# Kernel tuning notes

Measured on AMD Instinct MI355X. Metric: run time of the kernel, lower is better.

The kernel has to match this reference:

```python
import jax, jax.numpy as jnp
import numpy as np

NUM_PTS = 4
N_OFF = 4


def inverse_sigmoid(x, eps=1e-5):
    x = jnp.clip(x, 0.0, 1.0)
    return jnp.log(jnp.clip(x, eps, None) / jnp.clip(1.0 - x, eps, None))


def uniform_flat_indices(T, H, W, n):
    # torch: linspace(hop/2, D-1-hop/2, n).round().long(), meshed over (t,h,w)
    def ax(D):
        hop = D / n
        return jnp.round(jnp.linspace(hop / 2.0, D - 1.0 - hop / 2.0, n)).astype(jnp.int32)
    ti, hi, wi = ax(T), ax(H), ax(W)
    return ((ti[:, None, None] * H + hi[None, :, None]) * W + wi[None, None, :]).reshape(-1)


def _normalized_thw(idx, T, H, W):
    wn = (idx % W).astype(jnp.float32) / (W - 1)
    hn = ((idx // W) % H).astype(jnp.float32) / (H - 1)
    tn = (idx // (W * H)).astype(jnp.float32) / (T - 1)
    return jnp.stack([tn, hn, wn], axis=-1)


def grid_sample_3d(inp, grid):
    # Matches torch F.grid_sample 5D, bilinear, padding zeros, align_corners=False.
    # inp: (N,C,D,H,W); grid: (N,Do,Ho,Wo,3) with grid[...,0]=x->W, 1=y->H, 2=z->D
    N, C, D, H, W = inp.shape
    Do, Ho, Wo = grid.shape[1:4]
    P = Do * Ho * Wo
    g = grid.reshape(N, P, 3)
    ix = ((g[..., 0] + 1.0) * W - 1.0) * 0.5
    iy = ((g[..., 1] + 1.0) * H - 1.0) * 0.5
    iz = ((g[..., 2] + 1.0) * D - 1.0) * 0.5
    x0 = jnp.floor(ix); y0 = jnp.floor(iy); z0 = jnp.floor(iz)
    fx = ix - x0; fy = iy - y0; fz = iz - z0
    x0i = x0.astype(jnp.int32); y0i = y0.astype(jnp.int32); z0i = z0.astype(jnp.int32)
    inp_flat = inp.reshape(N, C, D * H * W)
    out = jnp.zeros((N, C, P), inp.dtype)
    for dz in (0, 1):
        for dy in (0, 1):
            for dx in (0, 1):
                xi = x0i + dx; yi = y0i + dy; zi = z0i + dz
                w = (fx if dx else 1.0 - fx) * (fy if dy else 1.0 - fy) * (fz if dz else 1.0 - fz)
                valid = (xi >= 0) & (xi < W) & (yi >= 0) & (yi < H) & (zi >= 0) & (zi < D)
                flat = (jnp.clip(zi, 0, D - 1) * H + jnp.clip(yi, 0, H - 1)) * W + jnp.clip(xi, 0, W - 1)
                vals = jnp.take_along_axis(inp_flat, jnp.broadcast_to(flat[:, None, :], (N, C, P)), axis=2)
                out = out + vals * (w * valid.astype(inp.dtype))[:, None, :]
    return out.reshape(N, C, Do, Ho, Wo)


def forward(features, pos, W1, b1, W2, b2, Wn, bn, Wl, bl, Woff, boff, Ww, bw, gamma, beta):
    B, C, T, H, Wd, L = features.shape
    THW = T * H * Wd
    No = N_OFF
    N = NUM_PTS ** 3
    d = C // No
    BLNo = B * L * No

    flat = uniform_flat_indices(T, H, Wd, NUM_PTS)                    # (N,)
    ind_pts = jnp.broadcast_to(flat[None, None, :], (B, L, N))

    feats_l = jnp.transpose(features, (0, 5, 2, 3, 4, 1)).reshape(B, L, THW, C)
    pos_l = jnp.transpose(pos, (0, 5, 2, 3, 4, 1)).reshape(B, L, THW, C)
    sampled_pts = feats_l[:, :, flat, :]                              # (B,L,N,C)
    sampled_pos = pos_l[:, :, flat, :]
    glob = jnp.transpose(jnp.mean(features, axis=(2, 3, 4)), (0, 2, 1))  # (B,L,C)
    glob = jnp.broadcast_to(glob[:, :, None, :], (B, L, N, C))

    off_src = jnp.concatenate([sampled_pts, sampled_pos, glob], axis=-1)
    off_src = jax.nn.relu(off_src @ W1 + b1)
    off_src = jax.nn.relu(off_src @ W2 + b2)                          # (B,L,N,C)

    nxt = off_src @ Wn + bn                                           # (B,L,N,3)
    w_l = jax.nn.softmax(off_src @ Wl + bl, axis=-1)                  # (B,L,N,L)

    osr = off_src.reshape(B, L, N, No, d).transpose(0, 1, 3, 2, 4).reshape(BLNo, N, d)
    offset = osr @ Woff + boff                                        # (BLNo,N,3)
    w_o = jax.nn.softmax(osr @ Ww + bw, axis=-1)[..., 1:]             # (BLNo,N,1)

    # --- build flow field: identity grid with sampled coords scattered in ---
    idx = jnp.broadcast_to(ind_pts[:, :, None, :], (B, L, No, N)).reshape(BLNo, N)
    thw = _normalized_thw(idx, T, H, Wd)
    samp = jax.nn.sigmoid(inverse_sigmoid(thw) + offset) * 2.0 - 1.0  # (BLNo,N,3)
    mesh = jnp.stack(jnp.meshgrid(jnp.linspace(-1.0, 1.0, T), jnp.linspace(-1.0, 1.0, H), jnp.linspace(-1.0, 1.0, Wd), indexing='ij'), axis=-1).reshape(THW, 3)
    base = jnp.broadcast_to(mesh[None], (BLNo, THW, 3))
    bI = jnp.arange(BLNo)[:, None]
    flow = base.at[bI, idx].set(samp).reshape(BLNo, T, H, Wd, 3)

    feats_rep = jnp.transpose(features, (0, 5, 1, 2, 3, 4))           # (B,L,C,T,H,W)
    feats_rep = jnp.broadcast_to(feats_rep[:, :, None], (B, L, No, C, T, H, Wd)).reshape(BLNo, C, T, H, Wd)
    sf = grid_sample_3d(feats_rep, flow)                              # (BLNo,C,T,H,W)
    sf = jnp.transpose(sf, (0, 2, 3, 4, 1))                           # (BLNo,T,H,W,C)

    wo_full = jnp.zeros((BLNo, THW, 1), features.dtype).at[bI, idx].set(w_o).reshape(BLNo, T, H, Wd, 1)
    wsf = (sf * wo_full).reshape(B, L, No, T, H, Wd, C).sum(axis=2)   # (B,L,T,H,W,C)
    feats2 = features + jnp.transpose(wsf, (0, 5, 2, 3, 4, 1))        # (B,C,T,H,W,L)

    # level weights scattered then summed over target-level axis l
    bI2 = jnp.arange(B)[:, None, None]
    lI2 = jnp.arange(L)[None, :, None]
    wl_full = jnp.zeros((B, L, THW, L), features.dtype).at[bI2, lI2, ind_pts].set(w_l)
    wl_sum = wl_full.sum(axis=-1).reshape(B, L, T, H, Wd)             # (B,L,T,H,W)
    feats3 = feats2 * jnp.transpose(wl_sum, (0, 2, 3, 4, 1))[:, None] # broadcast over C

    # LayerNorm over channel dim (transpose(1,-1) in torch)
    x = jnp.transpose(feats3, (0, 5, 2, 3, 4, 1))                     # (B,L,T,H,W,C)
    mu = jnp.mean(x, axis=-1, keepdims=True)
    var = jnp.var(x, axis=-1, keepdims=True)
    xn = (x - mu) * jax.lax.rsqrt(var + 1e-5) * gamma + beta
    feats_out = jnp.transpose(xn, (0, 5, 2, 3, 4, 1))

    # offset_adder -> next flattened indices
    thw2 = _normalized_thw(ind_pts, T, H, Wd)
    disp = jax.nn.sigmoid(inverse_sigmoid(thw2) + nxt)
    scale = jnp.array([T - 1, H - 1, Wd - 1], jnp.float32)
    di = jnp.round(disp * scale).astype(jnp.int32)
    next_ind = H * Wd * di[..., 0] + Wd * di[..., 1] + di[..., 2]
    return feats_out, next_ind


def setup_inputs():
    key = jax.random.key(0)
    ks = jax.random.split(key, 10)
    B, C, T, H, W, L = 1, 256, 8, 32, 32, 4
    s = 0.02
    d = C // N_OFF
    return {
        'features': jax.random.normal(ks[0], (B, C, T, H, W, L), jnp.float32),
        'pos': jax.random.normal(ks[1], (B, C, T, H, W, L), jnp.float32),
        'W1': jax.random.normal(ks[2], (3 * C, C), jnp.float32) * s,
        'b1': jnp.zeros((C,), jnp.float32),
        'W2': jax.random.normal(ks[3], (C, C), jnp.float32) * s,
        'b2': jnp.zeros((C,), jnp.float32),
        'Wn': jax.random.normal(ks[4], (C, 3), jnp.float32) * s,
        'bn': jnp.zeros((3,), jnp.float32),
        'Wl': jax.random.normal(ks[5], (C, L), jnp.float32) * s,
        'bl': jnp.zeros((L,), jnp.float32),
        'Woff': jax.random.normal(ks[6], (d, 3), jnp.float32) * s,
        'boff': jnp.zeros((3,), jnp.float32),
        'Ww': jax.random.normal(ks[7], (d, 2), jnp.float32) * s,
        'bw': jnp.zeros((2,), jnp.float32),
        'gamma': jnp.ones((C,), jnp.float32),
        'beta': jnp.zeros((C,), jnp.float32),
    }


def reference(features, pos, W1, b1, W2, b2, Wn, bn, Wl, bl, Woff, boff, Ww, bw, gamma, beta):
    return forward(features, pos, W1, b1, W2, b2, Wn, bn, Wl, bl, Woff, boff, Ww, bw, gamma, beta)
```

## Files before the change

### kernel.cpp

```cpp
#include <hip/hip_runtime.h>
#include <math.h>

#define CDIM 256
#define TDIM 8
#define HDIM 32
#define WDIM 32
#define LDIM 4
#define THW 8192
#define CSTR 32768
#define NS 64
#define OUT0_SIZE 8388608

#define K1 768
#define NS1 16
#define KB1 48
#define K2 256
#define NS2 16
#define KB2 16

__device__ __constant__ int c_ti[4] = {1, 3, 4, 6};
__device__ __constant__ int c_hw[4] = {4, 12, 19, 27};

__device__ __forceinline__ float sigm(float x) { return 1.f / (1.f + expf(-x)); }

__device__ __forceinline__ float wave_sum64(float x) {
#pragma unroll
    for (int s = 32; s > 0; s >>= 1) x += __shfl_xor(x, s, 64);
    return x;
}

__global__ void k_fill_glob(const float* __restrict__ feat, const float* __restrict__ beta,
                            float* __restrict__ out, float* __restrict__ glob) {
    int c = blockIdx.x;
    float b = beta[c];
    float4 bv = make_float4(b, b, b, b);
    const float4* f = (const float4*)(feat + (size_t)c * CSTR);
    float4* o = (float4*)(out + (size_t)c * CSTR);
    float4 a = make_float4(0.f, 0.f, 0.f, 0.f);
    for (int i = threadIdx.x; i < THW; i += 256) {
        float4 v = f[i];
        o[i] = bv;
        a.x += v.x; a.y += v.y; a.z += v.z; a.w += v.w;
    }
    __shared__ float4 sred[256];
    sred[threadIdx.x] = a;
    __syncthreads();
    for (int off = 128; off > 0; off >>= 1) {
        if (threadIdx.x < off) {
            float4 t = sred[threadIdx.x + off];
            sred[threadIdx.x].x += t.x; sred[threadIdx.x].y += t.y;
            sred[threadIdx.x].z += t.z; sred[threadIdx.x].w += t.w;
        }
        __syncthreads();
    }
    if (threadIdx.x == 0) {
        float4 t = sred[0];
        glob[0 * CDIM + c] = t.x * (1.f / 8192.f);
        glob[1 * CDIM + c] = t.y * (1.f / 8192.f);
        glob[2 * CDIM + c] = t.z * (1.f / 8192.f);
        glob[3 * CDIM + c] = t.w * (1.f / 8192.f);
    }
}

__global__ void k_gather(const float* __restrict__ feat, const float* __restrict__ pos,
                         const float* __restrict__ glob, float* __restrict__ in1) {
    int m = blockIdx.x;
    int l = m >> 6, n = m & 63;
    int sp = (c_ti[n >> 4] * HDIM + c_hw[(n >> 2) & 3]) * WDIM + c_hw[n & 3];
    for (int k = threadIdx.x; k < 768; k += 256) {
        float v;
        if (k < 256)      v = feat[(size_t)k * CSTR + sp * LDIM + l];
        else if (k < 512) v = pos[(size_t)(k - 256) * CSTR + sp * LDIM + l];
        else              v = glob[l * CDIM + (k - 512)];
        in1[m * 768 + k] = v;
    }
}

template <int K, int KB, int NKS>
__global__ void k_gemm_part(const float* __restrict__ A, const float* __restrict__ Wt,
                            float* __restrict__ part) {
    int mt = blockIdx.x / NKS, ks = blockIdx.x % NKS;
    int j = threadIdx.x;
    int m0 = mt * 16;
    const float* __restrict__ Arow = A + (size_t)m0 * K + ks * KB;
    const float* __restrict__ Wp = Wt + (size_t)(ks * KB) * 256 + j;
    float acc[16];
#pragma unroll
    for (int i = 0; i < 16; ++i) acc[i] = 0.f;
#pragma unroll 4
    for (int kk = 0; kk < KB; ++kk) {
        float wv = Wp[kk * 256];
#pragma unroll
        for (int i = 0; i < 16; ++i)
            acc[i] = fmaf(Arow[i * K + kk], wv, acc[i]);
    }
#pragma unroll
    for (int i = 0; i < 16; ++i)
        part[((size_t)(ks * 256 + m0 + i)) * 256 + j] = acc[i];
}

__global__ void k_h1red(const float* __restrict__ p1, const float* __restrict__ b1,
                        float* __restrict__ h1) {
    int m = blockIdx.x, k = threadIdx.x;
    float v = b1[k];
#pragma unroll
    for (int s = 0; s < NS1; ++s) v += p1[((size_t)(s * 256 + m)) * 256 + k];
    h1[m * 256 + k] = fmaxf(v, 0.f);
}

__global__ void k_heads(const float* __restrict__ p2, const float* __restrict__ b2,
                        const float* __restrict__ Wn, const float* __restrict__ bn,
                        const float* __restrict__ Woff, const float* __restrict__ boff,
                        const float* __restrict__ Ww, const float* __restrict__ bw,
                        float* __restrict__ samp, float* __restrict__ wo,
                        float* __restrict__ next_out) {
    __shared__ float redn[3][4];
    int m = blockIdx.x;
    int l = m >> 6, n = m & 63;
    int j = threadIdx.x;
    int o = j >> 6;
    int r = j & 63;

    float v = b2[j];
#pragma unroll
    for (int s = 0; s < NS2; ++s) v += p2[((size_t)(s * 256 + m)) * 256 + j];
    v = fmaxf(v, 0.f);

    float pn0 = wave_sum64(v * Wn[j * 3 + 0]);
    float pn1 = wave_sum64(v * Wn[j * 3 + 1]);
    float pn2 = wave_sum64(v * Wn[j * 3 + 2]);
    if (r == 0) { redn[0][o] = pn0; redn[1][o] = pn1; redn[2][o] = pn2; }

    float po0 = wave_sum64(v * Woff[r * 3 + 0]);
    float po1 = wave_sum64(v * Woff[r * 3 + 1]);
    float po2 = wave_sum64(v * Woff[r * 3 + 2]);
    float z0  = wave_sum64(v * Ww[r * 2 + 0]);
    float z1  = wave_sum64(v * Ww[r * 2 + 1]);

    float tn = (float)c_ti[n >> 4] / 7.f;
    float hn = (float)c_hw[(n >> 2) & 3] / 31.f;
    float wn = (float)c_hw[n & 3] / 31.f;
    float lg0 = logf(tn / (1.f - tn));
    float lg1 = logf(hn / (1.f - hn));
    float lg2 = logf(wn / (1.f - wn));

    if (r == 0) {
        int q = l * 4 + o;
        samp[(q * NS + n) * 3 + 0] = sigm(lg0 + po0 + boff[0]) * 2.f - 1.f;
        samp[(q * NS + n) * 3 + 1] = sigm(lg1 + po1 + boff[1]) * 2.f - 1.f;
        samp[(q * NS + n) * 3 + 2] = sigm(lg2 + po2 + boff[2]) * 2.f - 1.f;
        wo[q * NS + n] = 1.f / (1.f + expf((z0 + bw[0]) - (z1 + bw[1])));
    }
    __syncthreads();
    if (j == 0) {
        float t0 = redn[0][0] + redn[0][1] + redn[0][2] + redn[0][3];
        float t1 = redn[1][0] + redn[1][1] + redn[1][2] + redn[1][3];
        float t2 = redn[2][0] + redn[2][1] + redn[2][2] + redn[2][3];
        float d0 = rintf(sigm(lg0 + t0 + bn[0]) * 7.f);
        float d1 = rintf(sigm(lg1 + t1 + bn[1]) * 31.f);
        float d2 = rintf(sigm(lg2 + t2 + bn[2]) * 31.f);
        next_out[m] = 1024.f * d0 + 32.f * d1 + d2;
    }
}

__global__ void k_sample_ln(const float* __restrict__ feat,
                            const float* __restrict__ samp, const float* __restrict__ wo,
                            const float* __restrict__ gamma, const float* __restrict__ beta,
                            float* __restrict__ out) {
    __shared__ float s_w[32];
    __shared__ int s_o[32];
    __shared__ float red1[4], red2[4];
    int bm = blockIdx.x;
    int l = bm >> 6, n = bm & 63;
    int tid = threadIdx.x;

    if (tid < 4) {
        int o = tid, q = l * 4 + o;
        float wv = wo[q * NS + n];
        float g0 = samp[(q * NS + n) * 3 + 0];
        float g1 = samp[(q * NS + n) * 3 + 1];
        float g2 = samp[(q * NS + n) * 3 + 2];
        float ix = ((g0 + 1.f) * 32.f - 1.f) * 0.5f;
        float iy = ((g1 + 1.f) * 32.f - 1.f) * 0.5f;
        float iz = ((g2 + 1.f) * 8.f  - 1.f) * 0.5f;
        float x0f = floorf(ix), y0f = floorf(iy), z0f = floorf(iz);
        float fx = ix - x0f, fy = iy - y0f, fz = iz - z0f;
        int x0 = (int)x0f, y0 = (int)y0f, z0 = (int)z0f;
#pragma unroll
        for (int k = 0; k < 8; ++k) {
            int dx = k & 1, dy = (k >> 1) & 1, dz = k >> 2;
            int xi = x0 + dx, yi = y0 + dy, zi = z0 + dz;
            float w = (dx ? fx : 1.f - fx) * (dy ? fy : 1.f - fy) * (dz ? fz : 1.f - fz);
            bool valid = (xi >= 0) && (xi < WDIM) && (yi >= 0) && (yi < HDIM) && (zi >= 0) && (zi < TDIM);
            int xc = min(max(xi, 0), WDIM - 1);
            int yc = min(max(yi, 0), HDIM - 1);
            int zc = min(max(zi, 0), TDIM - 1);
            s_w[o * 8 + k] = valid ? w * wv : 0.f;
            s_o[o * 8 + k] = ((zc * HDIM + yc) * WDIM + xc) * LDIM + l;
        }
    }
    __syncthreads();

    int c = tid;
    const float* fc = feat + (size_t)c * CSTR;
    int sp = (c_ti[n >> 4] * HDIM + c_hw[(n >> 2) & 3]) * WDIM + c_hw[n & 3];
    float acc = fc[sp * LDIM + l];
#pragma unroll
    for (int k = 0; k < 32; ++k) acc += s_w[k] * fc[s_o[k]];

    float s1 = acc, s2 = acc * acc;
#pragma unroll
    for (int d = 32; d > 0; d >>= 1) { s1 += __shfl_xor(s1, d, 64); s2 += __shfl_xor(s2, d, 64); }
    int wid = tid >> 6;
    if ((tid & 63) == 0) { red1[wid] = s1; red2[wid] = s2; }
    __syncthreads();
    float tot  = red1[0] + red1[1] + red1[2] + red1[3];
    float totq = red2[0] + red2[1] + red2[2] + red2[3];
    float mu = tot * (1.f / 256.f);
    float var = fmaxf(totq * (1.f / 256.f) - mu * mu, 0.f);
    float y = (acc - mu) * rsqrtf(var + 1e-5f) * gamma[c] + beta[c];
    out[(size_t)c * CSTR + sp * LDIM + l] = y;
}

extern "C" void kernel_launch(void* const* d_in, const int* in_sizes, int n_in,
                              void* d_out, int out_size, void* d_ws, size_t ws_size,
                              hipStream_t stream) {
    const float* feat = (const float*)d_in[0];
    const float* pos  = (const float*)d_in[1];
    const float* W1   = (const float*)d_in[2];
    const float* b1   = (const float*)d_in[3];
    const float* W2   = (const float*)d_in[4];
    const float* b2   = (const float*)d_in[5];
    const float* Wn   = (const float*)d_in[6];
    const float* bn   = (const float*)d_in[7];
    const float* Woff = (const float*)d_in[10];
    const float* boff = (const float*)d_in[11];
    const float* Ww   = (const float*)d_in[12];
    const float* bw   = (const float*)d_in[13];
    const float* gamma= (const float*)d_in[14];
    const float* beta = (const float*)d_in[15];
    float* out = (float*)d_out;

    float* ws   = (float*)d_ws;
    float* glob = ws;
    float* in1  = glob + 1024;
    float* p1   = in1 + 196608;
    float* h1   = p1 + (NS1 * 65536);
    float* p2   = h1 + 65536;
    float* samp = p2 + (NS2 * 65536);
    float* wov  = samp + 3072;

    k_fill_glob<<<256, 256, 0, stream>>>(feat, beta, out, glob);
    k_gather<<<256, 256, 0, stream>>>(feat, pos, glob, in1);
    k_gemm_part<K1, KB1, NS1><<<16 * NS1, 256, 0, stream>>>(in1, W1, p1);
    k_h1red<<<256, 256, 0, stream>>>(p1, b1, h1);
    k_gemm_part<K2, KB2, NS2><<<16 * NS2, 256, 0, stream>>>(h1, W2, p2);
    k_heads<<<256, 256, 0, stream>>>(p2, b2, Wn, bn, Woff, boff, Ww, bw, samp, wov, out + OUT0_SIZE);
    k_sample_ln<<<256, 256, 0, stream>>>(feat, samp, wov, gamma, beta, out);
}
```

Measured before the change: 177.9 us.

## Fuse all stages into one cooperative kernel with grid-wide syncs

```diff
diff --git a/kernel.cpp b/kernel.cpp
--- a/kernel.cpp
+++ b/kernel.cpp
@@ -1,5 +1,8 @@
 #include <hip/hip_runtime.h>
+#include <hip/hip_cooperative_groups.h>
 #include <math.h>
+
+namespace cg = cooperative_groups;
 
 #define CDIM 256
 #define TDIM 8
@@ -11,13 +14,6 @@
 #define NS 64
 #define OUT0_SIZE 8388608
 
-#define K1 768
-#define NS1 16
-#define KB1 48
-#define K2 256
-#define NS2 16
-#define KB2 16
-
 __device__ __constant__ int c_ti[4] = {1, 3, 4, 6};
 __device__ __constant__ int c_hw[4] = {4, 12, 19, 27};
 
@@ -29,197 +25,209 @@
     return x;
 }
 
-__global__ void k_fill_glob(const float* __restrict__ feat, const float* __restrict__ beta,
-                            float* __restrict__ out, float* __restrict__ glob) {
-    int c = blockIdx.x;
-    float b = beta[c];
-    float4 bv = make_float4(b, b, b, b);
-    const float4* f = (const float4*)(feat + (size_t)c * CSTR);
-    float4* o = (float4*)(out + (size_t)c * CSTR);
-    float4 a = make_float4(0.f, 0.f, 0.f, 0.f);
-    for (int i = threadIdx.x; i < THW; i += 256) {
-        float4 v = f[i];
-        o[i] = bv;
-        a.x += v.x; a.y += v.y; a.z += v.z; a.w += v.w;
-    }
+__global__ void __launch_bounds__(256, 1)
+k_fused(const float* __restrict__ feat, const float* __restrict__ pos,
+        const float* __restrict__ W1, const float* __restrict__ b1,
+        const float* __restrict__ W2, const float* __restrict__ b2,
+        const float* __restrict__ Wn, const float* __restrict__ bn,
+        const float* __restrict__ Woff, const float* __restrict__ boff,
+        const float* __restrict__ Ww, const float* __restrict__ bw,
+        const float* __restrict__ gamma, const float* __restrict__ beta,
+        float* __restrict__ out, float* __restrict__ glob,
+        float* __restrict__ p1, float* __restrict__ p2,
+        float* __restrict__ next_out) {
+    cg::grid_group grid = cg::this_grid();
+    const int tid = threadIdx.x;
+    const int b = blockIdx.x;
+
     __shared__ float4 sred[256];
-    sred[threadIdx.x] = a;
-    __syncthreads();
-    for (int off = 128; off > 0; off >>= 1) {
-        if (threadIdx.x < off) {
-            float4 t = sred[threadIdx.x + off];
-            sred[threadIdx.x].x += t.x; sred[threadIdx.x].y += t.y;
-            sred[threadIdx.x].z += t.z; sred[threadIdx.x].w += t.w;
-        }
-        __syncthreads();
-    }
-    if (threadIdx.x == 0) {
-        float4 t = sred[0];
-        glob[0 * CDIM + c] = t.x * (1.f / 8192.f);
-        glob[1 * CDIM + c] = t.y * (1.f / 8192.f);
-        glob[2 * CDIM + c] = t.z * (1.f / 8192.f);
-        glob[3 * CDIM + c] = t.w * (1.f / 8192.f);
-    }
-}
-
-__global__ void k_gather(const float* __restrict__ feat, const float* __restrict__ pos,
-                         const float* __restrict__ glob, float* __restrict__ in1) {
-    int m = blockIdx.x;
-    int l = m >> 6, n = m & 63;
-    int sp = (c_ti[n >> 4] * HDIM + c_hw[(n >> 2) & 3]) * WDIM + c_hw[n & 3];
-    for (int k = threadIdx.x; k < 768; k += 256) {
-        float v;
-        if (k < 256)      v = feat[(size_t)k * CSTR + sp * LDIM + l];
-        else if (k < 512) v = pos[(size_t)(k - 256) * CSTR + sp * LDIM + l];
-        else              v = glob[l * CDIM + (k - 512)];
-        in1[m * 768 + k] = v;
-    }
-}
-
-template <int K, int KB, int NKS>
-__global__ void k_gemm_part(const float* __restrict__ A, const float* __restrict__ Wt,
-                            float* __restrict__ part) {
-    int mt = blockIdx.x / NKS, ks = blockIdx.x % NKS;
-    int j = threadIdx.x;
-    int m0 = mt * 16;
-    const float* __restrict__ Arow = A + (size_t)m0 * K + ks * KB;
-    const float* __restrict__ Wp = Wt + (size_t)(ks * KB) * 256 + j;
-    float acc[16];
-#pragma unroll
-    for (int i = 0; i < 16; ++i) acc[i] = 0.f;
+    __shared__ float sA[16][48];
+    __shared__ float sH[16][16];
+    __shared__ float s_samp[4][3];
+    __shared__ float s_wo[4];
+    __shared__ float s_w[32];
+    __shared__ int   s_o[32];
+    __shared__ float red1[4], red2[4], redn[3][4];
+
+    {
+        int c = b;
+        float bv = beta[c];
+        float4 bf = make_float4(bv, bv, bv, bv);
+        const float4* f = (const float4*)(feat + (size_t)c * CSTR);
+        float4* o = (float4*)(out + (size_t)c * CSTR);
+        float4 a = make_float4(0.f, 0.f, 0.f, 0.f);
+        for (int i = tid; i < THW; i += 256) {
+            float4 v = f[i];
+            o[i] = bf;
+            a.x += v.x; a.y += v.y; a.z += v.z; a.w += v.w;
+        }
+        sred[tid] = a;
+        __syncthreads();
+        for (int off = 128; off > 0; off >>= 1) {
+            if (tid < off) {
+                float4 t = sred[tid + off];
+                sred[tid].x += t.x; sred[tid].y += t.y;
+                sred[tid].z += t.z; sred[tid].w += t.w;
+            }
+            __syncthreads();
+        }
+        if (tid == 0) {
+            float4 t = sred[0];
+            glob[0 * CDIM + c] = t.x * (1.f / 8192.f);
+            glob[1 * CDIM + c] = t.y * (1.f / 8192.f);
+            glob[2 * CDIM + c] = t.z * (1.f / 8192.f);
+            glob[3 * CDIM + c] = t.w * (1.f / 8192.f);
+        }
+    }
+    grid.sync();
+
+    {
+        int mt = b >> 4, ks = b & 15;
+        for (int v = tid; v < 768; v += 256) {
+            int i = v / 48, kk = v - i * 48;
+            int k = ks * 48 + kk;
+            int m = mt * 16 + i, l = m >> 6, n = m & 63;
+            int sp = (c_ti[n >> 4] * HDIM + c_hw[(n >> 2) & 3]) * WDIM + c_hw[n & 3];
+            float val;
+            if (k < 256)      val = feat[(size_t)k * CSTR + sp * LDIM + l];
+            else if (k < 512) val = pos[(size_t)(k - 256) * CSTR + sp * LDIM + l];
+            else              val = glob[l * CDIM + (k - 512)];
+            sA[i][kk] = val;
+        }
+        __syncthreads();
+        int j = tid;
+        float acc[16];
+#pragma unroll
+        for (int i = 0; i < 16; ++i) acc[i] = 0.f;
 #pragma unroll 4
-    for (int kk = 0; kk < KB; ++kk) {
-        float wv = Wp[kk * 256];
+        for (int kk = 0; kk < 48; ++kk) {
+            float wv = W1[(size_t)(ks * 48 + kk) * 256 + j];
+#pragma unroll
+            for (int i = 0; i < 16; ++i) acc[i] = fmaf(sA[i][kk], wv, acc[i]);
+        }
 #pragma unroll
         for (int i = 0; i < 16; ++i)
-            acc[i] = fmaf(Arow[i * K + kk], wv, acc[i]);
-    }
-#pragma unroll
-    for (int i = 0; i < 16; ++i)
-        part[((size_t)(ks * 256 + m0 + i)) * 256 + j] = acc[i];
-}
-
-__global__ void k_h1red(const float* __restrict__ p1, const float* __restrict__ b1,
-                        float* __restrict__ h1) {
-    int m = blockIdx.x, k = threadIdx.x;
-    float v = b1[k];
-#pragma unroll
-    for (int s = 0; s < NS1; ++s) v += p1[((size_t)(s * 256 + m)) * 256 + k];
-    h1[m * 256 + k] = fmaxf(v, 0.f);
-}
-
-__global__ void k_heads(const float* __restrict__ p2, const float* __restrict__ b2,
-                        const float* __restrict__ Wn, const float* __restrict__ bn,
-                        const float* __restrict__ Woff, const float* __restrict__ boff,
-                        const float* __restrict__ Ww, const float* __restrict__ bw,
-                        float* __restrict__ samp, float* __restrict__ wo,
-                        float* __restrict__ next_out) {
-    __shared__ float redn[3][4];
-    int m = blockIdx.x;
-    int l = m >> 6, n = m & 63;
-    int j = threadIdx.x;
-    int o = j >> 6;
-    int r = j & 63;
-
-    float v = b2[j];
-#pragma unroll
-    for (int s = 0; s < NS2; ++s) v += p2[((size_t)(s * 256 + m)) * 256 + j];
-    v = fmaxf(v, 0.f);
-
-    float pn0 = wave_sum64(v * Wn[j * 3 + 0]);
-    float pn1 = wave_sum64(v * Wn[j * 3 + 1]);
-    float pn2 = wave_sum64(v * Wn[j * 3 + 2]);
-    if (r == 0) { redn[0][o] = pn0; redn[1][o] = pn1; redn[2][o] = pn2; }
-
-    float po0 = wave_sum64(v * Woff[r * 3 + 0]);
-    float po1 = wave_sum64(v * Woff[r * 3 + 1]);
-    float po2 = wave_sum64(v * Woff[r * 3 + 2]);
-    float z0  = wave_sum64(v * Ww[r * 2 + 0]);
-    float z1  = wave_sum64(v * Ww[r * 2 + 1]);
-
-    float tn = (float)c_ti[n >> 4] / 7.f;
-    float hn = (float)c_hw[(n >> 2) & 3] / 31.f;
-    float wn = (float)c_hw[n & 3] / 31.f;
-    float lg0 = logf(tn / (1.f - tn));
-    float lg1 = logf(hn / (1.f - hn));
-    float lg2 = logf(wn / (1.f - wn));
-
-    if (r == 0) {
-        int q = l * 4 + o;
-        samp[(q * NS + n) * 3 + 0] = sigm(lg0 + po0 + boff[0]) * 2.f - 1.f;
-        samp[(q * NS + n) * 3 + 1] = sigm(lg1 + po1 + boff[1]) * 2.f - 1.f;
-        samp[(q * NS + n) * 3 + 2] = sigm(lg2 + po2 + boff[2]) * 2.f - 1.f;
-        wo[q * NS + n] = 1.f / (1.f + expf((z0 + bw[0]) - (z1 + bw[1])));
-    }
-    __syncthreads();
-    if (j == 0) {
-        float t0 = redn[0][0] + redn[0][1] + redn[0][2] + redn[0][3];
-        float t1 = redn[1][0] + redn[1][1] + redn[1][2] + redn[1][3];
-        float t2 = redn[2][0] + redn[2][1] + redn[2][2] + redn[2][3];
-        float d0 = rintf(sigm(lg0 + t0 + bn[0]) * 7.f);
-        float d1 = rintf(sigm(lg1 + t1 + bn[1]) * 31.f);
-        float d2 = rintf(sigm(lg2 + t2 + bn[2]) * 31.f);
-        next_out[m] = 1024.f * d0 + 32.f * d1 + d2;
-    }
-}
-
-__global__ void k_sample_ln(const float* __restrict__ feat,
-                            const float* __restrict__ samp, const float* __restrict__ wo,
-                            const float* __restrict__ gamma, const float* __restrict__ beta,
-                            float* __restrict__ out) {
-    __shared__ float s_w[32];
-    __shared__ int s_o[32];
-    __shared__ float red1[4], red2[4];
-    int bm = blockIdx.x;
-    int l = bm >> 6, n = bm & 63;
-    int tid = threadIdx.x;
-
-    if (tid < 4) {
-        int o = tid, q = l * 4 + o;
-        float wv = wo[q * NS + n];
-        float g0 = samp[(q * NS + n) * 3 + 0];
-        float g1 = samp[(q * NS + n) * 3 + 1];
-        float g2 = samp[(q * NS + n) * 3 + 2];
-        float ix = ((g0 + 1.f) * 32.f - 1.f) * 0.5f;
-        float iy = ((g1 + 1.f) * 32.f - 1.f) * 0.5f;
-        float iz = ((g2 + 1.f) * 8.f  - 1.f) * 0.5f;
-        float x0f = floorf(ix), y0f = floorf(iy), z0f = floorf(iz);
-        float fx = ix - x0f, fy = iy - y0f, fz = iz - z0f;
-        int x0 = (int)x0f, y0 = (int)y0f, z0 = (int)z0f;
-#pragma unroll
-        for (int k = 0; k < 8; ++k) {
-            int dx = k & 1, dy = (k >> 1) & 1, dz = k >> 2;
-            int xi = x0 + dx, yi = y0 + dy, zi = z0 + dz;
-            float w = (dx ? fx : 1.f - fx) * (dy ? fy : 1.f - fy) * (dz ? fz : 1.f - fz);
-            bool valid = (xi >= 0) && (xi < WDIM) && (yi >= 0) && (yi < HDIM) && (zi >= 0) && (zi < TDIM);
-            int xc = min(max(xi, 0), WDIM - 1);
-            int yc = min(max(yi, 0), HDIM - 1);
-            int zc = min(max(zi, 0), TDIM - 1);
-            s_w[o * 8 + k] = valid ? w * wv : 0.f;
-            s_o[o * 8 + k] = ((zc * HDIM + yc) * WDIM + xc) * LDIM + l;
-        }
-    }
-    __syncthreads();
-
-    int c = tid;
-    const float* fc = feat + (size_t)c * CSTR;
-    int sp = (c_ti[n >> 4] * HDIM + c_hw[(n >> 2) & 3]) * WDIM + c_hw[n & 3];
-    float acc = fc[sp * LDIM + l];
-#pragma unroll
-    for (int k = 0; k < 32; ++k) acc += s_w[k] * fc[s_o[k]];
-
-    float s1 = acc, s2 = acc * acc;
-#pragma unroll
-    for (int d = 32; d > 0; d >>= 1) { s1 += __shfl_xor(s1, d, 64); s2 += __shfl_xor(s2, d, 64); }
-    int wid = tid >> 6;
-    if ((tid & 63) == 0) { red1[wid] = s1; red2[wid] = s2; }
-    __syncthreads();
-    float tot  = red1[0] + red1[1] + red1[2] + red1[3];
-    float totq = red2[0] + red2[1] + red2[2] + red2[3];
-    float mu = tot * (1.f / 256.f);
-    float var = fmaxf(totq * (1.f / 256.f) - mu * mu, 0.f);
-    float y = (acc - mu) * rsqrtf(var + 1e-5f) * gamma[c] + beta[c];
-    out[(size_t)c * CSTR + sp * LDIM + l] = y;
+            p1[((size_t)(ks * 256 + mt * 16 + i)) * 256 + j] = acc[i];
+    }
+    grid.sync();
+
+    {
+        int mt = b >> 4, ks = b & 15;
+        {
+            int i = tid >> 4, kk = tid & 15;
+            int m = mt * 16 + i, k = ks * 16 + kk;
+            float v = b1[k];
+#pragma unroll
+            for (int s = 0; s < 16; ++s) v += p1[((size_t)(s * 256 + m)) * 256 + k];
+            sH[i][kk] = fmaxf(v, 0.f);
+        }
+        __syncthreads();
+        int j = tid;
+        float acc[16];
+#pragma unroll
+        for (int i = 0; i < 16; ++i) acc[i] = 0.f;
+#pragma unroll
+        for (int kk = 0; kk < 16; ++kk) {
+            float wv = W2[(size_t)(ks * 16 + kk) * 256 + j];
+#pragma unroll
+            for (int i = 0; i < 16; ++i) acc[i] = fmaf(sH[i][kk], wv, acc[i]);
+        }
+#pragma unroll
+        for (int i = 0; i < 16; ++i)
+            p2[((size_t)(ks * 256 + mt * 16 + i)) * 256 + j] = acc[i];
+    }
+    grid.sync();
+
+    {
+        int m = b, l = m >> 6, n = m & 63;
+        int j = tid, o = j >> 6, r = j & 63;
+
+        float v = b2[j];
+#pragma unroll
+        for (int s = 0; s < 16; ++s) v += p2[((size_t)(s * 256 + m)) * 256 + j];
+        v = fmaxf(v, 0.f);
+
+        float pn0 = wave_sum64(v * Wn[j * 3 + 0]);
+        float pn1 = wave_sum64(v * Wn[j * 3 + 1]);
+        float pn2 = wave_sum64(v * Wn[j * 3 + 2]);
+        if (r == 0) { redn[0][o] = pn0; redn[1][o] = pn1; redn[2][o] = pn2; }
+
+        float po0 = wave_sum64(v * Woff[r * 3 + 0]);
+        float po1 = wave_sum64(v * Woff[r * 3 + 1]);
+        float po2 = wave_sum64(v * Woff[r * 3 + 2]);
+        float z0  = wave_sum64(v * Ww[r * 2 + 0]);
+        float z1  = wave_sum64(v * Ww[r * 2 + 1]);
+
+        float tn = (float)c_ti[n >> 4] / 7.f;
+        float hn = (float)c_hw[(n >> 2) & 3] / 31.f;
+        float wn = (float)c_hw[n & 3] / 31.f;
+        float lg0 = logf(tn / (1.f - tn));
+        float lg1 = logf(hn / (1.f - hn));
+        float lg2 = logf(wn / (1.f - wn));
+
+        if (r == 0) {
+            s_samp[o][0] = sigm(lg0 + po0 + boff[0]) * 2.f - 1.f;
+            s_samp[o][1] = sigm(lg1 + po1 + boff[1]) * 2.f - 1.f;
+            s_samp[o][2] = sigm(lg2 + po2 + boff[2]) * 2.f - 1.f;
+            s_wo[o] = 1.f / (1.f + expf((z0 + bw[0]) - (z1 + bw[1])));
+        }
+        __syncthreads();
+
+        if (tid == 0) {
+            float t0 = redn[0][0] + redn[0][1] + redn[0][2] + redn[0][3];
+            float t1 = redn[1][0] + redn[1][1] + redn[1][2] + redn[1][3];
+            float t2 = redn[2][0] + redn[2][1] + redn[2][2] + redn[2][3];
+            float d0 = rintf(sigm(lg0 + t0 + bn[0]) * 7.f);
+            float d1 = rintf(sigm(lg1 + t1 + bn[1]) * 31.f);
+            float d2 = rintf(sigm(lg2 + t2 + bn[2]) * 31.f);
+            next_out[m] = 1024.f * d0 + 32.f * d1 + d2;
+        }
+
+        if (tid < 4) {
+            int oo = tid;
+            float wv = s_wo[oo];
+            float g0 = s_samp[oo][0], g1 = s_samp[oo][1], g2 = s_samp[oo][2];
+            float ix = ((g0 + 1.f) * 32.f - 1.f) * 0.5f;
+            float iy = ((g1 + 1.f) * 32.f - 1.f) * 0.5f;
+            float iz = ((g2 + 1.f) * 8.f  - 1.f) * 0.5f;
+            float x0f = floorf(ix), y0f = floorf(iy), z0f = floorf(iz);
+            float fx = ix - x0f, fy = iy - y0f, fz = iz - z0f;
+            int x0 = (int)x0f, y0 = (int)y0f, z0 = (int)z0f;
+#pragma unroll
+            for (int k = 0; k < 8; ++k) {
+                int dx = k & 1, dy = (k >> 1) & 1, dz = k >> 2;
+                int xi = x0 + dx, yi = y0 + dy, zi = z0 + dz;
+                float w = (dx ? fx : 1.f - fx) * (dy ? fy : 1.f - fy) * (dz ? fz : 1.f - fz);
+                bool valid = (xi >= 0) && (xi < WDIM) && (yi >= 0) && (yi < HDIM) && (zi >= 0) && (zi < TDIM);
+                int xc = min(max(xi, 0), WDIM - 1);
+                int yc = min(max(yi, 0), HDIM - 1);
+                int zc = min(max(zi, 0), TDIM - 1);
+                s_w[oo * 8 + k] = valid ? w * wv : 0.f;
+                s_o[oo * 8 + k] = ((zc * HDIM + yc) * WDIM + xc) * LDIM + l;
+            }
+        }
+        __syncthreads();
+
+        int c = tid;
+        const float* fc = feat + (size_t)c * CSTR;
+        int sp = (c_ti[n >> 4] * HDIM + c_hw[(n >> 2) & 3]) * WDIM + c_hw[n & 3];
+        float acc = fc[sp * LDIM + l];
+#pragma unroll
+        for (int k = 0; k < 32; ++k) acc += s_w[k] * fc[s_o[k]];
+
+        float s1 = acc, s2 = acc * acc;
+#pragma unroll
+        for (int d = 32; d > 0; d >>= 1) { s1 += __shfl_xor(s1, d, 64); s2 += __shfl_xor(s2, d, 64); }
+        int wid = tid >> 6;
+        if ((tid & 63) == 0) { red1[wid] = s1; red2[wid] = s2; }
+        __syncthreads();
+        float tot  = red1[0] + red1[1] + red1[2] + red1[3];
+        float totq = red2[0] + red2[1] + red2[2] + red2[3];
+        float mu = tot * (1.f / 256.f);
+        float var = fmaxf(totq * (1.f / 256.f) - mu * mu, 0.f);
+        float y = (acc - mu) * rsqrtf(var + 1e-5f) * gamma[c] + beta[c];
+        out[(size_t)c * CSTR + sp * LDIM + l] = y;
+    }
 }
 
 extern "C" void kernel_launch(void* const* d_in, const int* in_sizes, int n_in,
@@ -240,21 +248,18 @@
     const float* gamma= (const float*)d_in[14];
     const float* beta = (const float*)d_in[15];
     float* out = (float*)d_out;
+    float* next_out = out + OUT0_SIZE;
 
     float* ws   = (float*)d_ws;
     float* glob = ws;
-    float* in1  = glob + 1024;
-    float* p1   = in1 + 196608;
-    float* h1   = p1 + (NS1 * 65536);
-    float* p2   = h1 + 65536;
-    float* samp = p2 + (NS2 * 65536);
-    float* wov  = samp + 3072;
-
-    k_fill_glob<<<256, 256, 0, stream>>>(feat, beta, out, glob);
-    k_gather<<<256, 256, 0, stream>>>(feat, pos, glob, in1);
-    k_gemm_part<K1, KB1, NS1><<<16 * NS1, 256, 0, stream>>>(in1, W1, p1);
-    k_h1red<<<256, 256, 0, stream>>>(p1, b1, h1);
-    k_gemm_part<K2, KB2, NS2><<<16 * NS2, 256, 0, stream>>>(h1, W2, p2);
-    k_heads<<<256, 256, 0, stream>>>(p2, b2, Wn, bn, Woff, boff, Ww, bw, samp, wov, out + OUT0_SIZE);
-    k_sample_ln<<<256, 256, 0, stream>>>(feat, samp, wov, gamma, beta, out);
+    float* p1   = glob + 1024;
+    float* p2   = p1 + 1048576;
+
+    void* args[] = {
+        (void*)&feat, (void*)&pos, (void*)&W1, (void*)&b1, (void*)&W2, (void*)&b2,
+        (void*)&Wn, (void*)&bn, (void*)&Woff, (void*)&boff, (void*)&Ww, (void*)&bw,
+        (void*)&gamma, (void*)&beta, (void*)&out, (void*)&glob, (void*)&p1, (void*)&p2,
+        (void*)&next_out
+    };
+    hipLaunchCooperativeKernel((void*)k_fused, dim3(256), dim3(256), args, 0, stream);
 }
```

Result: slower. 282.5 us (+58.8%).
